# Kernel optimization log

Measured on AMD Instinct MI355X. Metric: run time of the kernel, lower is better.

## Reference

```python
import jax, jax.numpy as jnp
import numpy as np
from jax import lax

B = 128; LEADS = 12; T = 1000; DM = 128; DI = 256; DS = 16; DR = 8; DC = 4; NB = 4; L = 199; OUT = 256


def _ln(x, g, b):
    m = x.mean(-1, keepdims=True)
    v = ((x - m) ** 2).mean(-1, keepdims=True)
    return (x - m) * lax.rsqrt(v + 1e-5) * g + b


def _ssm_scan(u, delta, A, Bm, Cm, D):
    """Selective scan. u, delta: [B,L,DI]; Bm, Cm: [B,L,DS]; A: [DI,DS]; D: [DI]."""
    def step(h, inp):
        d_t, B_t, C_t, u_t = inp  # [B,DI],[B,DS],[B,DS],[B,DI]
        dA = jnp.exp(d_t[:, :, None] * A[None])            # [B,DI,DS]
        h = dA * h + (d_t * u_t)[:, :, None] * B_t[:, None, :]
        y = jnp.einsum('bds,bs->bd', h, C_t)
        return h, y
    h0 = jnp.zeros((u.shape[0], A.shape[0], A.shape[1]), u.dtype)
    xs = (jnp.moveaxis(delta, 1, 0), jnp.moveaxis(Bm, 1, 0),
          jnp.moveaxis(Cm, 1, 0), jnp.moveaxis(u, 1, 0))
    _, ys = lax.scan(step, h0, xs)
    return jnp.moveaxis(ys, 0, 1) + u * D[None, None, :]


def setup_inputs() -> dict:
    key = jax.random.key(0)
    ks = jax.random.split(key, 16)
    n = lambda k, shp, s: jax.random.normal(k, shp, jnp.float32) * s
    inp = {}
    inp['x'] = jax.random.normal(ks[0], (B, LEADS, T), jnp.float32)
    inp['pe_w'] = n(ks[1], (DM, LEADS, 10), 0.1)
    inp['pe_b'] = jnp.zeros((DM,), jnp.float32)
    inp['gn_g'] = jnp.ones((DM,), jnp.float32)
    inp['gn_b'] = jnp.zeros((DM,), jnp.float32)
    inp['pos'] = n(ks[2], (1, L, DM), 0.02)
    inp['ln1_g'] = jnp.ones((NB, DM), jnp.float32)
    inp['ln1_b'] = jnp.zeros((NB, DM), jnp.float32)
    inp['in_w'] = n(ks[3], (NB, 2 * DI, DM), 0.05)
    inp['conv_w'] = n(ks[4], (NB, DI, DC), 0.2)
    inp['conv_b'] = jnp.zeros((NB, DI), jnp.float32)
    inp['xproj_w'] = n(ks[5], (NB, DR + 2 * DS, DI), 0.05)
    inp['dtproj_w'] = n(ks[6], (NB, DI, DR), 0.2)
    inp['dtproj_b'] = jnp.full((NB, DI), -4.6, jnp.float32)  # softplus(-4.6) ~= 0.01
    inp['A_log'] = jnp.tile(jnp.log(jnp.arange(1, DS + 1, dtype=jnp.float32))[None, None, :], (NB, DI, 1))
    inp['Dp'] = jnp.ones((NB, DI), jnp.float32)
    inp['outw'] = n(ks[7], (NB, DM, DI), 0.05)
    inp['ln2_g'] = jnp.ones((NB, DM), jnp.float32)
    inp['ln2_b'] = jnp.zeros((NB, DM), jnp.float32)
    inp['ffn_w1'] = n(ks[8], (NB, 4 * DM, DM), 0.05)
    inp['ffn_b1'] = jnp.zeros((NB, 4 * DM), jnp.float32)
    inp['ffn_w2'] = n(ks[9], (NB, DM, 4 * DM), 0.05)
    inp['ffn_b2'] = jnp.zeros((NB, DM), jnp.float32)
    inp['lnf_g'] = jnp.ones((DM,), jnp.float32)
    inp['lnf_b'] = jnp.zeros((DM,), jnp.float32)
    inp['head_w'] = n(ks[10], (OUT, DM), 0.05)
    inp['head_b'] = jnp.zeros((OUT,), jnp.float32)
    return inp


def reference(x, pe_w, pe_b, gn_g, gn_b, pos, ln1_g, ln1_b, in_w, conv_w, conv_b,
              xproj_w, dtproj_w, dtproj_b, A_log, Dp, outw, ln2_g, ln2_b,
              ffn_w1, ffn_b1, ffn_w2, ffn_b2, lnf_g, lnf_b, head_w, head_b):
    # --- patch embed: Conv1d(12 -> DM, k=10, s=5) + GroupNorm(8) + GELU ---
    h = lax.conv_general_dilated(x, pe_w, (5,), 'VALID',
                                 dimension_numbers=('NCH', 'OIH', 'NCH'))
    h = h + pe_b[None, :, None]                      # [B, DM, L]
    Bb, _, Lc = h.shape
    hg = h.reshape(Bb, 8, DM // 8, Lc)
    m = hg.mean((2, 3), keepdims=True)
    v = ((hg - m) ** 2).mean((2, 3), keepdims=True)
    h = ((hg - m) * lax.rsqrt(v + 1e-5)).reshape(Bb, DM, Lc)
    h = h * gn_g[None, :, None] + gn_b[None, :, None]
    h = jax.nn.gelu(h, approximate=False)
    h = jnp.swapaxes(h, 1, 2) + pos                  # [B, L, DM]

    for i in range(NB):
        # --- Mamba block ---
        u = _ln(h, ln1_g[i], ln1_b[i])
        xz = u @ in_w[i].T                           # [B, L, 2*DI]
        xm, z = jnp.split(xz, 2, axis=-1)
        xc = jnp.swapaxes(xm, 1, 2)                  # [B, DI, L]
        xc = jnp.pad(xc, ((0, 0), (0, 0), (DC - 1, 0)))  # causal pad
        xc = lax.conv_general_dilated(xc, conv_w[i][:, None, :], (1,), 'VALID',
                                      dimension_numbers=('NCH', 'OIH', 'NCH'),
                                      feature_group_count=DI)
        xc = xc + conv_b[i][None, :, None]
        u_ssm = jax.nn.silu(jnp.swapaxes(xc, 1, 2))  # [B, L, DI]
        dbl = u_ssm @ xproj_w[i].T                   # [B, L, DR+2*DS]
        dt, Bm, Cm = dbl[..., :DR], dbl[..., DR:DR + DS], dbl[..., DR + DS:]
        delta = jax.nn.softplus(dt @ dtproj_w[i].T + dtproj_b[i])  # [B, L, DI]
        A = -jnp.exp(A_log[i])                       # [DI, DS]
        y = _ssm_scan(u_ssm, delta, A, Bm, Cm, Dp[i])
        y = y * jax.nn.silu(z)
        h = h + y @ outw[i].T
        # --- FFN block ---
        f = _ln(h, ln2_g[i], ln2_b[i])
        f = jax.nn.gelu(f @ ffn_w1[i].T + ffn_b1[i], approximate=False)
        h = h + f @ ffn_w2[i].T + ffn_b2[i]

    h = _ln(h, lnf_g, lnf_b).mean(axis=1)            # [B, DM]
    return jax.nn.gelu(h @ head_w.T + head_b, approximate=False)  # [B, OUT]
```

## Files before the change

kernel.cpp:

```cpp
#include <hip/hip_runtime.h>
#include <math.h>

#define TOKS (128*199)
#define DM 128
#define DI 256
#define DS 16
#define DR 8
#define NBLK 4
#define LSEQ 199
#define BATCH 128

typedef __attribute__((ext_vector_type(8))) short bf16x8;
typedef __attribute__((ext_vector_type(4))) float f32x4;

__device__ __forceinline__ float gelu_f(float x) {
  return 0.5f * x * (1.0f + erff(x * 0.70710678118654752440f));
}
__device__ __forceinline__ float silu_fast(float x) {
  float e = __expf(-x);
  return x * __builtin_amdgcn_rcpf(1.0f + e);
}
__device__ __forceinline__ unsigned short f2bf(float f) {
  unsigned u = __float_as_uint(f);
  u += 0x7fffu + ((u >> 16) & 1u);
  return (unsigned short)(u >> 16);
}
__device__ __forceinline__ float bf2f(unsigned short h) {
  return __uint_as_float(((unsigned)h) << 16);
}

__global__ __launch_bounds__(256) void cvtw_kernel(const float* __restrict__ src,
                                                   unsigned short* __restrict__ dh,
                                                   unsigned short* __restrict__ dl, int n) {
  int i = blockIdx.x*256 + threadIdx.x;
  if (i < n) {
    float v = src[i];
    unsigned short h = f2bf(v);
    dh[i] = h;
    dl[i] = f2bf(v - bf2f(h));
  }
}
__global__ __launch_bounds__(256) void cvtw_pad_kernel(const float* __restrict__ src,
                                                       unsigned short* __restrict__ dh,
                                                       unsigned short* __restrict__ dl) {
  int i = blockIdx.x*256 + threadIdx.x;
  int blk = i >> 14, rem = i & 16383;
  int r = rem >> 8, c = rem & 255;
  float v = (r < 40) ? src[(size_t)blk*40*256 + r*256 + c] : 0.f;
  unsigned short h = f2bf(v);
  dh[i] = h;
  dl[i] = f2bf(v - bf2f(h));
}

__global__ __launch_bounds__(256) void pe_conv_kernel(
    const float* __restrict__ x, const float* __restrict__ pw,
    const float* __restrict__ pb, float* __restrict__ convo) {
  int b = blockIdx.x, tc = blockIdx.y;
  int t0 = tc * 25;
  int nt = (LSEQ - t0 < 25) ? (LSEQ - t0) : 25;
  __shared__ float sx[12][136];
  int tid = threadIdx.x;
  for (int i = tid; i < 12*136; i += 256) {
    int l = i / 136, k = i - l*136;
    int idx = t0*5 + k;
    sx[l][k] = (idx < 1000) ? x[(size_t)b*12000 + l*1000 + idx] : 0.f;
  }
  __syncthreads();
  for (int o = tid; o < DM*nt; o += 256) {
    int m = o / nt, tt = o - m*nt;
    const float* wr = pw + m*120;
    float acc = pb[m];
#pragma unroll
    for (int l = 0; l < 12; ++l) {
#pragma unroll
      for (int k = 0; k < 10; ++k)
        acc += sx[l][tt*5 + k] * wr[l*10 + k];
    }
    convo[((size_t)b*DM + m)*LSEQ + t0 + tt] = acc;
  }
}

__global__ void gn_kernel(const float* __restrict__ conv, const float* __restrict__ gg,
                          const float* __restrict__ gb, const float* __restrict__ pos,
                          float* __restrict__ h) {
  int b = blockIdx.x >> 3, grp = blockIdx.x & 7;
  const float* cb = conv + ((size_t)b*DM + grp*16)*LSEQ;
  int tid = threadIdx.x;
  float s = 0.f, s2 = 0.f;
  for (int i = tid; i < 16*LSEQ; i += 256) { float v = cb[i]; s += v; s2 += v*v; }
#pragma unroll
  for (int m = 1; m < 64; m <<= 1) { s += __shfl_xor(s, m); s2 += __shfl_xor(s2, m); }
  __shared__ float red[8];
  int lane = tid & 63, wid = tid >> 6;
  if (lane == 0) { red[wid] = s; red[4+wid] = s2; }
  __syncthreads();
  float S  = red[0]+red[1]+red[2]+red[3];
  float S2 = red[4]+red[5]+red[6]+red[7];
  const float inv = 1.0f/(16.0f*LSEQ);
  float mean = S*inv;
  float var  = S2*inv - mean*mean;
  float rstd = rsqrtf(var + 1e-5f);
  for (int i = tid; i < 16*LSEQ; i += 256) {
    int mloc = i / LSEQ; int t = i - mloc*LSEQ;
    int m = grp*16 + mloc;
    float v = (cb[i] - mean)*rstd*gg[m] + gb[m];
    v = gelu_f(v);
    h[((size_t)b*LSEQ + t)*DM + m] = v + pos[t*DM + m];
  }
}

__global__ void ln_kernel(const float* __restrict__ x, const float* __restrict__ g,
                          const float* __restrict__ bb,
                          unsigned short* __restrict__ oh, unsigned short* __restrict__ ol) {
  int tok = blockIdx.x*4 + (threadIdx.x >> 6);
  int lane = threadIdx.x & 63;
  const float* xr = x + (size_t)tok*DM;
  float v0 = xr[lane], v1 = xr[lane+64];
  float s = v0+v1, s2 = v0*v0+v1*v1;
#pragma unroll
  for (int m=1;m<64;m<<=1){ s += __shfl_xor(s,m); s2 += __shfl_xor(s2,m); }
  float mean = s*(1.f/DM);
  float var  = s2*(1.f/DM) - mean*mean;
  float rs = rsqrtf(var+1e-5f);
  float y0 = (v0-mean)*rs*g[lane]+bb[lane];
  float y1 = (v1-mean)*rs*g[lane+64]+bb[lane+64];
  size_t o0 = (size_t)tok*DM + lane;
  unsigned short h0 = f2bf(y0), h1 = f2bf(y1);
  oh[o0]    = h0; ol[o0]    = f2bf(y0 - bf2f(h0));
  oh[o0+64] = h1; ol[o0+64] = f2bf(y1 - bf2f(h1));
}

template<int NSUB, int MODE, int BIAS>
__global__ __launch_bounds__(256) void gemm_bf3(
    const unsigned short* __restrict__ Ah, const unsigned short* __restrict__ Al,
    const unsigned short* __restrict__ Wh, const unsigned short* __restrict__ Wl,
    const float* __restrict__ bias,
    float* __restrict__ Cf, unsigned short* __restrict__ Ch, unsigned short* __restrict__ Cl,
    float* __restrict__ Cf2, int N, int K) {
  constexpr int BN   = NSUB*32;
  constexpr int SZ   = 8192 + NSUB*2048;
  constexpr int WHOF = 8192;
  constexpr int WLOF = 8192 + NSUB*1024;
  __shared__ unsigned short lds[2][SZ];
  const int tid = threadIdx.x;
  const int w = tid >> 6, l = tid & 63;
  const int wm = w >> 1, wn = w & 1;
  const int fr = l & 15, fq = l >> 4;
  const size_t bm0 = (size_t)blockIdx.y * 128;
  const size_t bn0 = (size_t)blockIdx.x * BN;
  const size_t lane_off = (size_t)(l >> 2)*K + (size_t)(((l & 3) ^ ((l >> 3) & 3)) * 8);
  const unsigned short* gAh = Ah + bm0*K + lane_off + (size_t)w*16*K;
  const unsigned short* gAl = Al + bm0*K + lane_off + (size_t)w*16*K;
  const unsigned short* gWh = Wh + bn0*K + lane_off + (size_t)w*16*K;
  const unsigned short* gWl = Wl + bn0*K + lane_off + (size_t)w*16*K;
  const size_t c4 = (size_t)4*16*K;

  f32x4 acc[4][NSUB];
#pragma unroll
  for (int m=0;m<4;++m)
#pragma unroll
    for (int n=0;n<NSUB;++n) acc[m][n] = (f32x4){0.f,0.f,0.f,0.f};

#define STAGE(BUF, KO) do { \
    unsigned short* bb_ = lds[BUF]; \
    __builtin_amdgcn_global_load_lds(gAh + (KO),      &bb_[w*512],              16, 0, 0); \
    __builtin_amdgcn_global_load_lds(gAh + c4 + (KO), &bb_[(w+4)*512],          16, 0, 0); \
    __builtin_amdgcn_global_load_lds(gAl + (KO),      &bb_[4096 + w*512],       16, 0, 0); \
    __builtin_amdgcn_global_load_lds(gAl + c4 + (KO), &bb_[4096 + (w+4)*512],   16, 0, 0); \
    __builtin_amdgcn_global_load_lds(gWh + (KO),      &bb_[WHOF + w*512],       16, 0, 0); \
    __builtin_amdgcn_global_load_lds(gWl + (KO),      &bb_[WLOF + w*512],       16, 0, 0); \
    if (NSUB == 4) { \
      __builtin_amdgcn_global_load_lds(gWh + c4 + (KO), &bb_[WHOF + (w+4)*512], 16, 0, 0); \
      __builtin_amdgcn_global_load_lds(gWl + c4 + (KO), &bb_[WLOF + (w+4)*512], 16, 0, 0); \
    } \
  } while (0)

  int cur = 0;
  STAGE(0, 0);
  for (int k0 = 0; k0 < K; k0 += 32) {
    __syncthreads();
    if (k0 + 32 < K) STAGE(cur ^ 1, k0 + 32);
    const unsigned short* b = lds[cur];
    bf16x8 whf[NSUB], wlf[NSUB];
#pragma unroll
    for (int n=0;n<NSUB;++n) {
      int row = wn*(NSUB*16) + n*16 + fr;
      int off = row*32 + ((fq ^ ((row>>1)&3))*8);
      whf[n] = *(const bf16x8*)&b[WHOF + off];
      wlf[n] = *(const bf16x8*)&b[WLOF + off];
    }
#pragma unroll
    for (int m=0;m<4;++m) {
      int row = wm*64 + m*16 + fr;
      int off = row*32 + ((fq ^ ((row>>1)&3))*8);
      bf16x8 ah = *(const bf16x8*)&b[off];
      bf16x8 al = *(const bf16x8*)&b[4096 + off];
#pragma unroll
      for (int n=0;n<NSUB;++n) {
        acc[m][n] = __builtin_amdgcn_mfma_f32_16x16x32_bf16(ah, whf[n], acc[m][n], 0, 0, 0);
        acc[m][n] = __builtin_amdgcn_mfma_f32_16x16x32_bf16(al, whf[n], acc[m][n], 0, 0, 0);
        acc[m][n] = __builtin_amdgcn_mfma_f32_16x16x32_bf16(ah, wlf[n], acc[m][n], 0, 0, 0);
      }
    }
    cur ^= 1;
  }
#undef STAGE

#pragma unroll
  for (int m=0;m<4;++m) {
#pragma unroll
    for (int n=0;n<NSUB;++n) {
      int col = (int)bn0 + wn*(NSUB*16) + n*16 + fr;
      float bv = BIAS ? bias[col] : 0.f;
#pragma unroll
      for (int v=0;v<4;++v) {
        float val = acc[m][n][v] + bv;
        size_t row = bm0 + wm*64 + m*16 + fq*4 + v;
        if (MODE == 0) {
          Cf[row*N + col] = val;
        } else if (MODE == 1) {
          Cf[row*N + col] += val;
        } else if (MODE == 2) {
          val = gelu_f(val);
          unsigned short hh = f2bf(val);
          Ch[row*N + col] = hh;
          Cl[row*N + col] = f2bf(val - bf2f(hh));
        } else {
          if (col < 256) Cf[row*256 + col] = val;
          else           Cf2[row*256 + (col-256)] = silu_fast(val);
        }
      }
    }
  }
}

__global__ void dwconv_kernel(const float* __restrict__ X, const float* __restrict__ w,
                              const float* __restrict__ bias, float* __restrict__ uss,
                              unsigned short* __restrict__ ussh, unsigned short* __restrict__ ussl) {
  int tok = blockIdx.x;
  int d = threadIdx.x;
  int t = tok % LSEQ;
  float4 wv = *(const float4*)(w + d*4);
  float acc = bias[d];
  const float* xp = X + (size_t)tok*DI + d;
  if (t >= 3) acc += xp[-3*DI]*wv.x;
  if (t >= 2) acc += xp[-2*DI]*wv.y;
  if (t >= 1) acc += xp[-1*DI]*wv.z;
  acc += xp[0]*wv.w;
  float sv = silu_fast(acc);
  size_t o = (size_t)tok*DI + d;
  uss[o] = sv;
  unsigned short hh = f2bf(sv);
  ussh[o] = hh;
  ussl[o] = f2bf(sv - bf2f(hh));
}

__global__ __launch_bounds__(256) void dtproj_kernel(
    const float* __restrict__ dbl, const float* __restrict__ dtw,
    const float* __restrict__ dtb, float* __restrict__ dlt) {
  int tok0 = blockIdx.x * 8;
  int d = threadIdx.x;
  __shared__ float sdt[8][DR];
  if (d < 64) sdt[d >> 3][d & 7] = dbl[(size_t)(tok0 + (d >> 3))*64 + (d & 7)];
  float wreg[DR];
#pragma unroll
  for (int rr = 0; rr < DR; ++rr) wreg[rr] = dtw[d*DR + rr];
  float b0 = dtb[d];
  __syncthreads();
#pragma unroll
  for (int tt = 0; tt < 8; ++tt) {
    float acc = b0;
#pragma unroll
    for (int rr = 0; rr < DR; ++rr) acc += sdt[tt][rr]*wreg[rr];
    acc = (acc > 20.f) ? acc : log1pf(__expf(acc));
    dlt[(size_t)(tok0 + tt)*DI + d] = acc;
  }
}

__global__ __launch_bounds__(256) void scan_kernel(
    const float* __restrict__ uss, const float* __restrict__ dlt,
    const float* __restrict__ dbl,
    const float* __restrict__ A_log, const float* __restrict__ Dp,
    const float* __restrict__ GZ,
    unsigned short* __restrict__ yh, unsigned short* __restrict__ yl) {
  int bg = blockIdx.x;
  int b = bg >> 4, dg = bg & 15;
  int tid = threadIdx.x;
  int s = tid & 15, dloc = tid >> 4;
  int d = dg*16 + dloc;
  float As = -__expf(A_log[d*DS + s]);
  float Dd = Dp[d];
  float h = 0.f;
  size_t tokbase = (size_t)b*LSEQ;
  const float* pdt = dlt + tokbase*DI + d;
  const float* pu  = uss + tokbase*DI + d;
  const float* pgz = GZ  + tokbase*DI + d;
  const float* pB  = dbl + tokbase*64 + 8  + s;
  const float* pC  = pB + 16;
  unsigned short* pyh = yh + tokbase*DI + d;
  unsigned short* pyl = yl + tokbase*DI + d;
#pragma unroll 4
  for (int t = 0; t < LSEQ; ++t) {
    float dt = pdt[(size_t)t*DI];
    float u  = pu [(size_t)t*DI];
    float Bv = pB [t*64];
    float Cv = pC [t*64];
    float dA = __expf(dt*As);
    h = fmaf(dA, h, dt*u*Bv);
    float p = h*Cv;
    p += __shfl_xor(p, 1);
    p += __shfl_xor(p, 2);
    p += __shfl_xor(p, 4);
    p += __shfl_xor(p, 8);
    if (s == 0) {
      float gz = pgz[(size_t)t*DI];
      float yv = fmaf(u, Dd, p) * gz;
      unsigned short hh = f2bf(yv);
      pyh[(size_t)t*DI] = hh;
      pyl[(size_t)t*DI] = f2bf(yv - bf2f(hh));
    }
  }
}

__global__ void final_kernel(const float* __restrict__ h, const float* __restrict__ g,
                             const float* __restrict__ bta, const float* __restrict__ hw,
                             const float* __restrict__ hb, float* __restrict__ out) {
  int b = blockIdx.x;
  int tid = threadIdx.x, lane = tid & 63, wid = tid >> 6;
  float s0 = 0.f, s1 = 0.f;
  for (int t = wid; t < LSEQ; t += 4) {
    const float* hr = h + ((size_t)b*LSEQ + t)*DM;
    float v0 = hr[lane], v1 = hr[lane+64];
    float ss = v0+v1, ss2 = v0*v0+v1*v1;
#pragma unroll
    for (int m=1;m<64;m<<=1){ ss += __shfl_xor(ss,m); ss2 += __shfl_xor(ss2,m); }
    float mean = ss*(1.f/DM);
    float var  = ss2*(1.f/DM)-mean*mean;
    float rs = rsqrtf(var+1e-5f);
    s0 += (v0-mean)*rs*g[lane]+bta[lane];
    s1 += (v1-mean)*rs*g[lane+64]+bta[lane+64];
  }
  __shared__ float sm[4][128];
  sm[wid][lane] = s0; sm[wid][lane+64] = s1;
  __syncthreads();
  __shared__ float mv[128];
  if (tid < 128) mv[tid] = (sm[0][tid]+sm[1][tid]+sm[2][tid]+sm[3][tid]) * (1.f/199.f);
  __syncthreads();
  int j = tid;
  const float* wr = hw + (size_t)j*DM;
  float acc = hb[j];
#pragma unroll 4
  for (int k=0;k<DM;k++) acc += mv[k]*wr[k];
  out[(size_t)b*256 + j] = gelu_f(acc);
}

extern "C" void kernel_launch(void* const* d_in, const int* in_sizes, int n_in,
                              void* d_out, int out_size, void* d_ws, size_t ws_size,
                              hipStream_t stream) {
  const float* x       = (const float*)d_in[0];
  const float* pe_w    = (const float*)d_in[1];
  const float* pe_b    = (const float*)d_in[2];
  const float* gn_g    = (const float*)d_in[3];
  const float* gn_b    = (const float*)d_in[4];
  const float* pos     = (const float*)d_in[5];
  const float* ln1_g   = (const float*)d_in[6];
  const float* ln1_b   = (const float*)d_in[7];
  const float* in_w    = (const float*)d_in[8];
  const float* conv_w  = (const float*)d_in[9];
  const float* conv_b  = (const float*)d_in[10];
  const float* xproj_w = (const float*)d_in[11];
  const float* dtproj_w= (const float*)d_in[12];
  const float* dtproj_b= (const float*)d_in[13];
  const float* A_log   = (const float*)d_in[14];
  const float* Dp      = (const float*)d_in[15];
  const float* outw    = (const float*)d_in[16];
  const float* ln2_g   = (const float*)d_in[17];
  const float* ln2_b   = (const float*)d_in[18];
  const float* ffn_w1  = (const float*)d_in[19];
  const float* ffn_b1  = (const float*)d_in[20];
  const float* ffn_w2  = (const float*)d_in[21];
  const float* ffn_b2  = (const float*)d_in[22];
  const float* lnf_g   = (const float*)d_in[23];
  const float* lnf_b   = (const float*)d_in[24];
  const float* head_w  = (const float*)d_in[25];
  const float* head_b  = (const float*)d_in[26];
  float* out = (float*)d_out;

  float* ws  = (float*)d_ws;
  float* h    = ws;
  float* X    = h   + (size_t)TOKS*DM;
  float* Z    = X   + (size_t)TOKS*DI;
  float* uss  = Z   + (size_t)TOKS*DI;
  float* dlt  = uss + (size_t)TOKS*DI;
  float* dbl  = dlt + (size_t)TOKS*DI;
  unsigned short* uh   = (unsigned short*)(dbl + (size_t)TOKS*64);
  unsigned short* ul   = uh   + (size_t)TOKS*DM;
  unsigned short* ussh = ul   + (size_t)TOKS*DM;
  unsigned short* ussl = ussh + (size_t)TOKS*DI;
  unsigned short* wb   = ussl + (size_t)TOKS*DI;
  unsigned short* inwh = wb;
  unsigned short* inwl = inwh + 262144;
  unsigned short* xpwh = inwl + 262144;
  unsigned short* xpwl = xpwh + 65536;
  unsigned short* outwh= xpwl + 65536;
  unsigned short* outwl= outwh + 131072;
  unsigned short* w1h  = outwl + 131072;
  unsigned short* w1l  = w1h + 262144;
  unsigned short* w2h  = w1l + 262144;
  unsigned short* w2l  = w2h + 262144;
  unsigned short* yh   = (unsigned short*)X;
  unsigned short* yl   = yh + (size_t)TOKS*DI;
  unsigned short* f1h  = (unsigned short*)uss;
  unsigned short* f1l  = f1h + (size_t)TOKS*512;

  cvtw_kernel<<<1024, 256, 0, stream>>>(in_w,   inwh, inwl, 262144);
  cvtw_pad_kernel<<<256, 256, 0, stream>>>(xproj_w, xpwh, xpwl);
  cvtw_kernel<<<512, 256, 0, stream>>>(outw,   outwh, outwl, 131072);
  cvtw_kernel<<<1024, 256, 0, stream>>>(ffn_w1, w1h, w1l, 262144);
  cvtw_kernel<<<1024, 256, 0, stream>>>(ffn_w2, w2h, w2l, 262144);

  pe_conv_kernel<<<dim3(BATCH, 8), 256, 0, stream>>>(x, pe_w, pe_b, X);
  gn_kernel<<<BATCH*8, 256, 0, stream>>>(X, gn_g, gn_b, pos, h);

  for (int i = 0; i < NBLK; ++i) {
    ln_kernel<<<TOKS/4, 256, 0, stream>>>(h, ln1_g + i*DM, ln1_b + i*DM, uh, ul);
    gemm_bf3<4,3,0><<<dim3(4, 199), 256, 0, stream>>>(
        uh, ul, inwh + (size_t)i*65536, inwl + (size_t)i*65536,
        nullptr, X, nullptr, nullptr, Z, 512, DM);
    dwconv_kernel<<<TOKS, 256, 0, stream>>>(X, conv_w + i*DI*4, conv_b + i*DI,
                                            uss, ussh, ussl);
    gemm_bf3<2,0,0><<<dim3(1, 199), 256, 0, stream>>>(
        ussh, ussl, xpwh + (size_t)i*16384, xpwl + (size_t)i*16384,
        nullptr, dbl, nullptr, nullptr, nullptr, 64, DI);
    dtproj_kernel<<<TOKS/8, 256, 0, stream>>>(
        dbl, dtproj_w + (size_t)i*DI*DR, dtproj_b + i*DI, dlt);
    scan_kernel<<<BATCH*16, 256, 0, stream>>>(
        uss, dlt, dbl, A_log + (size_t)i*DI*DS, Dp + i*DI, Z, yh, yl);
    gemm_bf3<4,1,0><<<dim3(1, 199), 256, 0, stream>>>(
        yh, yl, outwh + (size_t)i*32768, outwl + (size_t)i*32768,
        nullptr, h, nullptr, nullptr, nullptr, DM, DI);
    ln_kernel<<<TOKS/4, 256, 0, stream>>>(h, ln2_g + i*DM, ln2_b + i*DM, uh, ul);
    gemm_bf3<4,2,1><<<dim3(4, 199), 256, 0, stream>>>(
        uh, ul, w1h + (size_t)i*65536, w1l + (size_t)i*65536,
        ffn_b1 + i*512, nullptr, f1h, f1l, nullptr, 512, DM);
    gemm_bf3<4,1,1><<<dim3(1, 199), 256, 0, stream>>>(
        f1h, f1l, w2h + (size_t)i*65536, w2l + (size_t)i*65536,
        ffn_b2 + i*DM, h, nullptr, nullptr, nullptr, DM, 512);
  }

  final_kernel<<<BATCH, 256, 0, stream>>>(h, lnf_g, lnf_b, head_w, head_b, out);
}
```

Measured before the change: 1.639 ms.

## Keep full SSM state per thread in scan, prefetch inputs two steps ahead

The selective scan now gives each thread one channel and holds all 16 state entries in registers, instead of spreading the state dimension across 16 lanes and reducing with shuffles. The per-step dt, u and gate loads are software-pipelined two timesteps ahead, and B/C are read as wave-uniform broadcast loads. This removes the shuffle reduction and the lane-divergent store, and cuts redundant loads of dt/u. The cost is a much smaller grid (512 waves of 64 threads) with a longer serial chain per thread, which may under-occupy the GPU.

```diff
diff --git a/kernel.cpp b/kernel.cpp
--- a/kernel.cpp
+++ b/kernel.cpp
@@ -277,48 +277,45 @@
   }
 }
 
-__global__ __launch_bounds__(256) void scan_kernel(
+__global__ __launch_bounds__(64) void scan_kernel(
     const float* __restrict__ uss, const float* __restrict__ dlt,
     const float* __restrict__ dbl,
     const float* __restrict__ A_log, const float* __restrict__ Dp,
     const float* __restrict__ GZ,
     unsigned short* __restrict__ yh, unsigned short* __restrict__ yl) {
-  int bg = blockIdx.x;
-  int b = bg >> 4, dg = bg & 15;
-  int tid = threadIdx.x;
-  int s = tid & 15, dloc = tid >> 4;
-  int d = dg*16 + dloc;
-  float As = -__expf(A_log[d*DS + s]);
+  int b = blockIdx.x;
+  int d = blockIdx.y*64 + threadIdx.x;
+  float A[DS], hreg[DS];
+#pragma unroll
+  for (int s=0;s<DS;++s) { A[s] = -__expf(A_log[d*DS + s]); hreg[s] = 0.f; }
   float Dd = Dp[d];
-  float h = 0.f;
   size_t tokbase = (size_t)b*LSEQ;
   const float* pdt = dlt + tokbase*DI + d;
   const float* pu  = uss + tokbase*DI + d;
   const float* pgz = GZ  + tokbase*DI + d;
-  const float* pB  = dbl + tokbase*64 + 8  + s;
-  const float* pC  = pB + 16;
+  const float* pbc = dbl + tokbase*64;
   unsigned short* pyh = yh + tokbase*DI + d;
   unsigned short* pyl = yl + tokbase*DI + d;
-#pragma unroll 4
+  float dt0 = pdt[0],          u0 = pu[0],          g0 = pgz[0];
+  float dt1 = pdt[DI],         u1 = pu[DI],         g1 = pgz[DI];
   for (int t = 0; t < LSEQ; ++t) {
-    float dt = pdt[(size_t)t*DI];
-    float u  = pu [(size_t)t*DI];
-    float Bv = pB [t*64];
-    float Cv = pC [t*64];
-    float dA = __expf(dt*As);
-    h = fmaf(dA, h, dt*u*Bv);
-    float p = h*Cv;
-    p += __shfl_xor(p, 1);
-    p += __shfl_xor(p, 2);
-    p += __shfl_xor(p, 4);
-    p += __shfl_xor(p, 8);
-    if (s == 0) {
-      float gz = pgz[(size_t)t*DI];
-      float yv = fmaf(u, Dd, p) * gz;
-      unsigned short hh = f2bf(yv);
-      pyh[(size_t)t*DI] = hh;
-      pyl[(size_t)t*DI] = f2bf(yv - bf2f(hh));
+    float dt = dt0, u = u0, gz = g0;
+    dt0 = dt1; u0 = u1; g0 = g1;
+    int tp = (t + 2 < LSEQ) ? t + 2 : LSEQ - 1;
+    dt1 = pdt[(size_t)tp*DI]; u1 = pu[(size_t)tp*DI]; g1 = pgz[(size_t)tp*DI];
+    const float* bc = pbc + (size_t)t*64;
+    float du = dt*u;
+    float yv = u*Dd;
+#pragma unroll
+    for (int s=0;s<DS;++s) {
+      float dA = __expf(dt*A[s]);
+      hreg[s] = fmaf(dA, hreg[s], du*bc[8+s]);
+      yv = fmaf(hreg[s], bc[24+s], yv);
     }
+    yv *= gz;
+    unsigned short hh = f2bf(yv);
+    pyh[(size_t)t*DI] = hh;
+    pyl[(size_t)t*DI] = f2bf(yv - bf2f(hh));
   }
 }
 
@@ -434,7 +431,7 @@
         nullptr, dbl, nullptr, nullptr, nullptr, 64, DI);
     dtproj_kernel<<<TOKS/8, 256, 0, stream>>>(
         dbl, dtproj_w + (size_t)i*DI*DR, dtproj_b + i*DI, dlt);
-    scan_kernel<<<BATCH*16, 256, 0, stream>>>(
+    scan_kernel<<<dim3(BATCH, 4), 64, 0, stream>>>(
         uss, dlt, dbl, A_log + (size_t)i*DI*DS, Dp + i*DI, Z, yh, yl);
     gemm_bf3<4,1,0><<<dim3(1, 199), 256, 0, stream>>>(
         yh, yl, outwh + (size_t)i*32768, outwl + (size_t)i*32768,
```

After: 1.578 ms. 3.7% less time.
